# Kernel tuning notes

Measured on AMD Instinct MI355X. Metric: run time of the kernel, lower is better.

Reference implementation:

```python
import jax, jax.numpy as jnp
import numpy as np

H = 1024   # hidden_size
NH = 32    # num_heads
D = H // NH  # head_dim = 32
M = 2      # num_timescales
BMIN, BMAX = 0.85, 0.9995
EPS = 1e-6
ROPE_BASE = 10000.0
LN_EPS = 1e-5


def setup_inputs() -> dict:
    key = jax.random.key(0)
    ks = jax.random.split(key, 8)
    b, t = 4, 1024
    x = jax.random.normal(ks[0], (b, t, H), jnp.float32)
    # xavier-uniform for q/k/v/out (matches _reset_parameters)
    sc = (6.0 / (H + H)) ** 0.5
    Wq = jax.random.uniform(ks[1], (H, H), jnp.float32, -sc, sc)
    Wk = jax.random.uniform(ks[2], (H, H), jnp.float32, -sc, sc)
    Wv = jax.random.uniform(ks[3], (H, H), jnp.float32, -sc, sc)
    Wout = jax.random.uniform(ks[4], (H, H), jnp.float32, -sc, sc)
    bout = jnp.zeros((H,), jnp.float32)
    # beta_proj: random weight, bias set so sigmoid(bias) = linspace(beta_min, beta_max)
    scb = (6.0 / (H + NH * M)) ** 0.5
    Wbeta = jax.random.uniform(ks[5], (NH * M, H), jnp.float32, -scb, scb)
    targets = jnp.linspace(BMIN, BMAX, M)
    bbeta = jnp.tile(jnp.log(targets / (1.0 - targets)), NH)  # repeat 'm -> (h m)'
    # mix_proj initialized to zeros (uniform mixing via softmax)
    Wmix = jnp.zeros((NH * M, H), jnp.float32)
    bmix = jnp.zeros((NH * M,), jnp.float32)
    ln_g = jnp.ones((H,), jnp.float32)
    ln_b = jnp.zeros((H,), jnp.float32)
    return dict(x=x, Wq=Wq, Wk=Wk, Wv=Wv, Wbeta=Wbeta, bbeta=bbeta,
                Wmix=Wmix, bmix=bmix, Wout=Wout, bout=bout, ln_g=ln_g, ln_b=ln_b)


def _rope(u, cos, sin):
    # u: [b,t,h,d] with d even; cos/sin: [1,t,1,d//2]
    half = D // 2
    u1, u2 = u[..., :half], u[..., half:]
    return jnp.concatenate([u1 * cos - u2 * sin, u1 * sin + u2 * cos], axis=-1)


def _forward(x, Wq, Wk, Wv, Wbeta, bbeta, Wmix, bmix, Wout, bout, ln_g, ln_b):
    b, t, _ = x.shape
    q = (x @ Wq.T).reshape(b, t, NH, D)
    k = (x @ Wk.T).reshape(b, t, NH, D)
    v = (x @ Wv.T).reshape(b, t, NH, D)
    # RoPE cache
    half = D // 2
    inv_freq = 1.0 / (ROPE_BASE ** (jnp.arange(half, dtype=jnp.float32) / half))
    freqs = jnp.arange(t, dtype=jnp.float32)[:, None] * inv_freq  # [t,half]
    cos = jnp.cos(freqs)[None, :, None, :]
    sin = jnp.sin(freqs)[None, :, None, :]
    q = _rope(q, cos, sin)
    k = _rope(k, cos, sin)
    phi_q = jax.nn.elu(q) + 1.0
    phi_k = jax.nn.elu(k) + 1.0
    beta = jnp.clip(jax.nn.sigmoid((x @ Wbeta.T + bbeta).reshape(b, t, NH, M)), BMIN, BMAX)
    mix = jax.nn.softmax((x @ Wmix.T + bmix).reshape(b, t, NH, M), axis=-1)

    def step(carry, xs):
        S, K = carry  # S:[b,h,M,d,d]  K:[b,h,M,d]
        pq, pk, vt, bt, mt = xs  # [b,h,d],[b,h,d],[b,h,d],[b,h,M],[b,h,M]
        K = K * bt[..., None] + pk[:, :, None, :]
        S = S * bt[..., None, None] + pk[:, :, None, :, None] * vt[:, :, None, None, :]
        num = jnp.einsum('bhd,bhmdc->bhmc', pq, S)
        den = jnp.einsum('bhd,bhmd->bhm', pq, K) + EPS
        y = jnp.sum(num / den[..., None] * mt[..., None], axis=2)  # [b,h,d]
        return (S, K), y

    S0 = jnp.zeros((b, NH, M, D, D), x.dtype)
    K0 = jnp.zeros((b, NH, M, D), x.dtype)
    tf = lambda a: jnp.moveaxis(a, 1, 0)  # time-major for scan
    _, ys = jax.lax.scan(step, (S0, K0), (tf(phi_q), tf(phi_k), tf(v), tf(beta), tf(mix)))
    y = jnp.moveaxis(ys, 0, 1).reshape(b, t, H) @ Wout.T + bout
    z = x + y  # residual; dropout is identity in eval
    mu = z.mean(-1, keepdims=True)
    var = ((z - mu) ** 2).mean(-1, keepdims=True)
    return (z - mu) / jnp.sqrt(var + LN_EPS) * ln_g + ln_b


def reference(x, Wq, Wk, Wv, Wbeta, bbeta, Wmix, bmix, Wout, bout, ln_g, ln_b):
    return _forward(x, Wq, Wk, Wv, Wbeta, bbeta, Wmix, bmix, Wout, bout, ln_g, ln_b)
```

## Files before the change

kernel.cpp:

```cpp
#include <hip/hip_runtime.h>
#include <math.h>

#define TT 1024
#define BB 4
#define HH 1024
#define NHH 32
#define CL 64
#define NCH (TT/CL)

typedef unsigned short u16;
typedef __attribute__((ext_vector_type(8))) short short8;
typedef __attribute__((ext_vector_type(8))) unsigned short u16x8;
typedef __attribute__((ext_vector_type(4))) float floatx4;

__device__ __forceinline__ float sigmoidf_(float x){ return 1.f/(1.f+expf(-x)); }
__device__ __forceinline__ u16 f2b(float f){
  union { float f; unsigned u; } x; x.f = f;
  unsigned r = x.u + 0x7FFFu + ((x.u >> 16) & 1u);
  return (u16)(r >> 16);
}
__device__ __forceinline__ float b2f(u16 v){
  union { unsigned u; float f; } x; x.u = ((unsigned)v) << 16;
  return x.f;
}

__global__ __launch_bounds__(256) void cast_all_k(
    const float* __restrict__ x, const float* __restrict__ Wq, const float* __restrict__ Wk,
    const float* __restrict__ Wv, const float* __restrict__ Wbeta, const float* __restrict__ Wmix,
    const float* __restrict__ Wout,
    u16* __restrict__ x_bf, u16* __restrict__ Wf, u16* __restrict__ Wout_bf,
    float* __restrict__ ct, float* __restrict__ st)
{
  int gid = blockIdx.x*256 + threadIdx.x;
  if (gid < 16384) {
    int t = gid >> 4, j = gid & 15;
    float invf = powf(10000.f, -(float)j/16.f);
    float ang = (float)t * invf;
    ct[gid] = cosf(ang);
    st[gid] = sinf(ang);
  }
  size_t e = (size_t)gid*4;
  const float* src; u16* dst; size_t so, dof;
  if      (e < 4194304) { src=x;     dst=x_bf;    so=e;          dof=so; }
  else if (e < 5242880) { src=Wq;    dst=Wf;      so=e-4194304;  dof=so; }
  else if (e < 6291456) { src=Wk;    dst=Wf;      so=e-5242880;  dof=so+1048576; }
  else if (e < 7340032) { src=Wv;    dst=Wf;      so=e-6291456;  dof=so+2097152; }
  else if (e < 7405568) { src=Wbeta; dst=Wf;      so=e-7340032;  dof=so+3145728; }
  else if (e < 7471104) { src=Wmix;  dst=Wf;      so=e-7405568;  dof=so+3211264; }
  else                  { src=Wout;  dst=Wout_bf; so=e-7471104;  dof=so; }
  float4 f = *reinterpret_cast<const float4*>(src + so);
  ushort4 u; u.x=f2b(f.x); u.y=f2b(f.y); u.z=f2b(f.z); u.w=f2b(f.w);
  *reinterpret_cast<ushort4*>(dst + dof) = u;
}

__global__ __launch_bounds__(256) void gemm_qkv_k(
    const u16* __restrict__ A, const u16* __restrict__ W,
    const float* __restrict__ ct, const float* __restrict__ st,
    const float* __restrict__ bbeta, const float* __restrict__ bmix,
    u16* __restrict__ qkv, float* __restrict__ betag, float* __restrict__ mixg)
{
  __shared__ u16 As[128*64];
  __shared__ u16 Ws[128*64];
  const int tid = threadIdx.x;
  const int lane = tid & 63;
  const int wave = tid >> 6;
  const int wm = wave >> 1, wn = wave & 1;
  const int id = blockIdx.x;
  const int row0 = (id & 31)*128, bx = id >> 5, col0 = bx*128;
  const int lr = lane & 15, lkg = lane >> 4;

  floatx4 acc[4][4];
  #pragma unroll
  for (int mt=0; mt<4; ++mt)
    #pragma unroll
    for (int nt=0; nt<4; ++nt)
      acc[mt][nt] = (floatx4){0.f,0.f,0.f,0.f};

  for (int k0 = 0; k0 < 1024; k0 += 64) {
    __syncthreads();
    #pragma unroll
    for (int it = 0; it < 4; ++it) {
      int li  = it*256 + tid;
      int row = li >> 3, ckp = li & 7;
      int ck  = ckp ^ (row & 7);
      const u16* ga = A + (size_t)(row0+row)*1024 + k0 + ck*8;
      const u16* gw = W + (size_t)(col0+row)*1024 + k0 + ck*8;
      __builtin_amdgcn_global_load_lds(
          (const __attribute__((address_space(1))) void*)ga,
          (__attribute__((address_space(3))) void*)(As + (size_t)(li & ~63)*8), 16, 0, 0);
      __builtin_amdgcn_global_load_lds(
          (const __attribute__((address_space(1))) void*)gw,
          (__attribute__((address_space(3))) void*)(Ws + (size_t)(li & ~63)*8), 16, 0, 0);
    }
    __syncthreads();
    #pragma unroll
    for (int kk = 0; kk < 64; kk += 32) {
      short8 af[4], wf[4];
      const int ckw = (kk >> 3) + lkg;
      #pragma unroll
      for (int t = 0; t < 4; ++t) {
        int rowA = wm*64 + t*16 + lr;
        int rowW = wn*64 + t*16 + lr;
        af[t] = *reinterpret_cast<const short8*>(As + rowA*64 + (ckw ^ (rowA & 7))*8);
        wf[t] = *reinterpret_cast<const short8*>(Ws + rowW*64 + (ckw ^ (rowW & 7))*8);
      }
      #pragma unroll
      for (int mt = 0; mt < 4; ++mt)
        #pragma unroll
        for (int nt = 0; nt < 4; ++nt)
          acc[mt][nt] = __builtin_amdgcn_mfma_f32_16x16x32_bf16(af[mt], wf[nt], acc[mt][nt], 0, 0, 0);
    }
  }
  if (bx < 16) {
    #pragma unroll
    for (int mt = 0; mt < 4; ++mt) {
      #pragma unroll
      for (int r = 0; r < 4; ++r) {
        int row = row0 + wm*64 + mt*16 + lkg*4 + r;
        int t = row & (TT-1);
        float c_ = ct[t*16 + lr], s_ = st[t*16 + lr];
        #pragma unroll
        for (int nt = 0; nt < 4; nt += 2) {
          float u1 = acc[mt][nt][r], u2 = acc[mt][nt+1][r];
          float r1 = u1*c_ - u2*s_;
          float r2 = u1*s_ + u2*c_;
          r1 = r1 > 0.f ? r1+1.f : expf(r1);
          r2 = r2 > 0.f ? r2+1.f : expf(r2);
          int col = col0 + wn*64 + nt*16 + lr;
          qkv[(size_t)row*3072 + col]      = f2b(r1);
          qkv[(size_t)row*3072 + col + 16] = f2b(r2);
        }
      }
    }
  } else if (bx < 24) {
    #pragma unroll
    for (int mt = 0; mt < 4; ++mt)
      #pragma unroll
      for (int r = 0; r < 4; ++r) {
        int row = row0 + wm*64 + mt*16 + lkg*4 + r;
        #pragma unroll
        for (int nt = 0; nt < 4; ++nt) {
          int col = col0 + wn*64 + nt*16 + lr;
          qkv[(size_t)row*3072 + col] = f2b(acc[mt][nt][r]);
        }
      }
  } else {
    #pragma unroll
    for (int mt = 0; mt < 4; ++mt)
      #pragma unroll
      for (int r = 0; r < 4; ++r) {
        int row = row0 + wm*64 + mt*16 + lkg*4 + r;
        #pragma unroll
        for (int nt = 0; nt < 4; ++nt) {
          int cidx = nt*16 + lr;
          float v = acc[mt][nt][r];
          if (wn == 0) {
            float bv = sigmoidf_(v + bbeta[cidx]);
            betag[(size_t)row*64 + cidx] = fminf(fmaxf(bv, 0.85f), 0.9995f);
          } else {
            float a = v + bmix[cidx];
            float o = __shfl_xor(a, 1);
            float e = expf(a - fmaxf(a, o));
            float es = e + __shfl_xor(e, 1);
            mixg[(size_t)row*64 + cidx] = e/es;
          }
        }
      }
  }
}

__global__ __launch_bounds__(256) void gemm_out_k(
    const u16* __restrict__ A, const u16* __restrict__ W,
    float* __restrict__ Zp0, float* __restrict__ Zp1)
{
  __shared__ u16 As[128*64];
  __shared__ u16 Ws[128*64];
  const int tid = threadIdx.x;
  const int lane = tid & 63;
  const int wave = tid >> 6;
  const int wm = wave >> 1, wn = wave & 1;
  const int id = blockIdx.x;
  const int row0 = (id & 31)*128, col0 = ((id >> 5) & 7)*128, kh = id >> 8;
  float* Z = kh ? Zp1 : Zp0;
  const int lr = lane & 15, lkg = lane >> 4;
  floatx4 acc[4][4];
  #pragma unroll
  for (int mt=0; mt<4; ++mt)
    #pragma unroll
    for (int nt=0; nt<4; ++nt)
      acc[mt][nt] = (floatx4){0.f,0.f,0.f,0.f};
  for (int k0 = kh*512; k0 < kh*512 + 512; k0 += 64) {
    __syncthreads();
    #pragma unroll
    for (int it = 0; it < 4; ++it) {
      int li  = it*256 + tid;
      int row = li >> 3, ckp = li & 7;
      int ck  = ckp ^ (row & 7);
      const u16* ga = A + (size_t)(row0+row)*1024 + k0 + ck*8;
      const u16* gw = W + (size_t)(col0+row)*1024 + k0 + ck*8;
      __builtin_amdgcn_global_load_lds(
          (const __attribute__((address_space(1))) void*)ga,
          (__attribute__((address_space(3))) void*)(As + (size_t)(li & ~63)*8), 16, 0, 0);
      __builtin_amdgcn_global_load_lds(
          (const __attribute__((address_space(1))) void*)gw,
          (__attribute__((address_space(3))) void*)(Ws + (size_t)(li & ~63)*8), 16, 0, 0);
    }
    __syncthreads();
    #pragma unroll
    for (int kk = 0; kk < 64; kk += 32) {
      short8 af[4], wf[4];
      const int ckw = (kk >> 3) + lkg;
      #pragma unroll
      for (int t = 0; t < 4; ++t) {
        int rowA = wm*64 + t*16 + lr;
        int rowW = wn*64 + t*16 + lr;
        af[t] = *reinterpret_cast<const short8*>(As + rowA*64 + (ckw ^ (rowA & 7))*8);
        wf[t] = *reinterpret_cast<const short8*>(Ws + rowW*64 + (ckw ^ (rowW & 7))*8);
      }
      #pragma unroll
      for (int mt = 0; mt < 4; ++mt)
        #pragma unroll
        for (int nt = 0; nt < 4; ++nt)
          acc[mt][nt] = __builtin_amdgcn_mfma_f32_16x16x32_bf16(af[mt], wf[nt], acc[mt][nt], 0, 0, 0);
    }
  }
  #pragma unroll
  for (int mt = 0; mt < 4; ++mt)
    #pragma unroll
    for (int r = 0; r < 4; ++r) {
      int row = row0 + wm*64 + mt*16 + lkg*4 + r;
      #pragma unroll
      for (int nt = 0; nt < 4; ++nt) {
        int col = col0 + wn*64 + nt*16 + lr;
        Z[(size_t)row*HH + col] = acc[mt][nt][r];
      }
    }
}

__global__ __launch_bounds__(256) void scan_delta_k(
    const u16* __restrict__ qkv, const float* __restrict__ betag,
    float* __restrict__ dS, float* __restrict__ dK,
    float* __restrict__ pLg, float* __restrict__ pg)
{
  __shared__ __align__(16) u16 K2T[2][32][72];
  __shared__ __align__(16) u16 VT[32][72];
  __shared__ float bets[2][64], pbuf[2][64], wjs[2][64], pLs[2];
  const int ch = blockIdx.x, h = blockIdx.y, b = blockIdx.z;
  const int bh = b*NHH + h;
  const int tid = threadIdx.x;
  const int t0 = ch*CL;
  const int j = tid >> 2, oct = tid & 3;
  size_t rowbase = (size_t)(b*TT + t0 + j)*3072 + h*32 + oct*8;
  u16x8 k8 = *reinterpret_cast<const u16x8*>(qkv + rowbase + 1024);
  u16x8 v8 = *reinterpret_cast<const u16x8*>(qkv + rowbase + 2048);
  if (tid < 128) {
    int m = tid & 1, tl = tid >> 1;
    bets[m][tl] = betag[(size_t)(b*TT + t0 + tl)*64 + h*2 + m];
  }
  #pragma unroll
  for (int dd = 0; dd < 8; ++dd) VT[oct*8+dd][j] = v8[dd];
  __syncthreads();
  if (tid < 128) {
    int m = tid >> 6, l = tid & 63;
    float p = bets[m][l];
    #pragma unroll
    for (int off = 1; off < 64; off <<= 1) {
      float o = __shfl_up(p, off);
      if (l >= off) p *= o;
    }
    pbuf[m][l] = p;
    if (l == 63) pLs[m] = p;
  }
  __syncthreads();
  if (tid < 128) {
    int m = tid >> 6, l = tid & 63;
    wjs[m][l] = pLs[m] / pbuf[m][l];
    pg[(((size_t)bh*NCH + ch)*2 + m)*64 + l] = pbuf[m][l];
  }
  if (tid < 2) pLg[((size_t)bh*NCH + ch)*2 + tid] = pLs[tid];
  __syncthreads();
  float w0 = wjs[0][j], w1 = wjs[1][j];
  #pragma unroll
  for (int dd = 0; dd < 8; ++dd) {
    float kv = b2f(k8[dd]);
    K2T[0][oct*8+dd][j] = f2b(kv*w0);
    K2T[1][oct*8+dd][j] = f2b(kv*w1);
  }
  __syncthreads();
  {
    const int wv = tid >> 6, lane = tid & 63, lr = lane & 15, kg = lane >> 4;
    const int m = wv >> 1, mt = wv & 1;
    floatx4 a0 = (floatx4){0.f,0.f,0.f,0.f}, a1 = (floatx4){0.f,0.f,0.f,0.f};
    #pragma unroll
    for (int ks = 0; ks < 2; ++ks) {
      short8 af = *reinterpret_cast<const short8*>(&K2T[m][mt*16 + lr][ks*32 + kg*8]);
      short8 b0 = *reinterpret_cast<const short8*>(&VT[lr][ks*32 + kg*8]);
      short8 b1 = *reinterpret_cast<const short8*>(&VT[16 + lr][ks*32 + kg*8]);
      a0 = __builtin_amdgcn_mfma_f32_16x16x32_bf16(af, b0, a0, 0, 0, 0);
      a1 = __builtin_amdgcn_mfma_f32_16x16x32_bf16(af, b1, a1, 0, 0, 0);
    }
    size_t base = (((size_t)bh*NCH + ch)*2 + m)*1024;
    #pragma unroll
    for (int r = 0; r < 4; ++r) {
      int d = mt*16 + kg*4 + r;
      dS[base + d*32 + lr]      = a0[r];
      dS[base + d*32 + 16 + lr] = a1[r];
    }
  }
  if (tid < 64) {
    int m = tid >> 5, d = tid & 31;
    float s = 0.f;
    #pragma unroll
    for (int g = 0; g < 8; ++g) {
      u16x8 kk = *reinterpret_cast<const u16x8*>(&K2T[m][d][g*8]);
      #pragma unroll
      for (int dd = 0; dd < 8; ++dd) s += b2f(kk[dd]);
    }
    dK[(((size_t)bh*NCH + ch)*2 + m)*32 + d] = s;
  }
}

__global__ __launch_bounds__(256) void scan_state_k(
    float* dSS0, float* dKK0, const float* __restrict__ pLg)
{
  const int bhm = blockIdx.x >> 2, part = blockIdx.x & 3;
  const int bh = bhm >> 1, m = bhm & 1;
  const int idx = part*256 + threadIdx.x;
  float pls[NCH], dv[NCH];
  #pragma unroll
  for (int ch = 0; ch < NCH; ++ch) pls[ch] = pLg[((size_t)bh*NCH + ch)*2 + m];
  #pragma unroll
  for (int ch = 0; ch < NCH; ++ch) dv[ch] = dSS0[(((size_t)bh*NCH + ch)*2 + m)*1024 + idx];
  float S = 0.f;
  #pragma unroll
  for (int ch = 0; ch < NCH; ++ch) {
    dSS0[(((size_t)bh*NCH + ch)*2 + m)*1024 + idx] = S;
    S = fmaf(pls[ch], S, dv[ch]);
  }
  if (part == 0 && threadIdx.x < 32) {
    int d = threadIdx.x;
    float kv[NCH];
    #pragma unroll
    for (int ch = 0; ch < NCH; ++ch) kv[ch] = dKK0[(((size_t)bh*NCH + ch)*2 + m)*32 + d];
    float K0 = 0.f;
    #pragma unroll
    for (int ch = 0; ch < NCH; ++ch) {
      dKK0[(((size_t)bh*NCH + ch)*2 + m)*32 + d] = K0;
      K0 = fmaf(pls[ch], K0, kv[ch]);
    }
  }
}

__global__ __launch_bounds__(256) void scan_apply_k(
    const u16* __restrict__ qkv, const float* __restrict__ mixg,
    const float* __restrict__ S0g, const float* __restrict__ K0g,
    const float* __restrict__ pg, u16* __restrict__ yb)
{
  __shared__ __align__(16) u16 Qs[64][32], Ks[64][32];
  __shared__ __align__(16) u16 VT[32][72];
  __shared__ __align__(16) u16 At[2][64][72];
  __shared__ __align__(16) u16 S0T[2][2][32][40];
  __shared__ float K0s[2][32];
  __shared__ float pbv[2][64], ipb[2][64], mixs[2][64], coef[2][64];
  const int ch = blockIdx.x, h = blockIdx.y, b = blockIdx.z;
  const int bh = b*NHH + h;
  const int tid = threadIdx.x;
  const int t0 = ch*CL;
  {
    int j = tid >> 2, oct = tid & 3;
    size_t rb = (size_t)(b*TT + t0 + j)*3072 + h*32 + oct*8;
    u16x8 q8 = *reinterpret_cast<const u16x8*>(qkv + rb);
    u16x8 k8 = *reinterpret_cast<const u16x8*>(qkv + rb + 1024);
    u16x8 v8 = *reinterpret_cast<const u16x8*>(qkv + rb + 2048);
    *reinterpret_cast<u16x8*>(&Qs[j][oct*8]) = q8;
    *reinterpret_cast<u16x8*>(&Ks[j][oct*8]) = k8;
    #pragma unroll
    for (int dd = 0; dd < 8; ++dd) VT[oct*8+dd][j] = v8[dd];
  }
  for (int u = tid; u < 2048; u += 256) {
    int m = u >> 10, r = u & 1023, d = r >> 5, c = r & 31;
    float val = S0g[(((size_t)bh*NCH + ch)*2 + m)*1024 + r];
    u16 hv = f2b(val);
    float lo = val - b2f(hv);
    S0T[m][0][c][d] = hv;
    S0T[m][1][c][d] = f2b(lo);
  }
  if (tid < 64) {
    int m = tid >> 5, d = tid & 31;
    K0s[m][d] = K0g[(((size_t)bh*NCH + ch)*2 + m)*32 + d];
  }
  if (tid < 128) {
    int m = tid & 1, i = tid >> 1;
    float p = pg[(((size_t)bh*NCH + ch)*2 + m)*64 + i];
    pbv[m][i] = p;
    ipb[m][i] = 1.f/p;
  } else if (tid < 192) {
    int i = tid - 128;
    size_t rb = (size_t)(b*TT + t0 + i)*64 + h*2;
    mixs[0][i] = mixg[rb];
    mixs[1][i] = mixg[rb+1];
  }
  __syncthreads();
  {
    const int wv = tid >> 6, lane = tid & 63, lr = lane & 15, kg = lane >> 4;
    short8 aq = *reinterpret_cast<const short8*>(&Qs[wv*16 + lr][kg*8]);
    #pragma unroll
    for (int nt = 0; nt < 4; ++nt) {
      short8 bk = *reinterpret_cast<const short8*>(&Ks[nt*16 + lr][kg*8]);
      floatx4 a0 = (floatx4){0.f,0.f,0.f,0.f};
      a0 = __builtin_amdgcn_mfma_f32_16x16x32_bf16(aq, bk, a0, 0, 0, 0);
      int jg = nt*16 + lr;
      float ip0 = ipb[0][jg], ip1 = ipb[1][jg];
      #pragma unroll
      for (int r = 0; r < 4; ++r) {
        int ig = wv*16 + kg*4 + r;
        float val = a0[r];
        bool ok = (jg <= ig);
        At[0][ig][jg] = f2b(ok ? val*ip0 : 0.f);
        At[1][ig][jg] = f2b(ok ? val*ip1 : 0.f);
      }
    }
  }
  __syncthreads();
  if (tid < 128) {
    int m = tid & 1, i = tid >> 1;
    float qK0 = 0.f;
    #pragma unroll
    for (int g = 0; g < 4; ++g) {
      u16x8 qq = *reinterpret_cast<const u16x8*>(&Qs[i][g*8]);
      #pragma unroll
      for (int dd = 0; dd < 8; ++dd) qK0 = fmaf(b2f(qq[dd]), K0s[m][g*8+dd], qK0);
    }
    float As_ = 0.f;
    #pragma unroll
    for (int g = 0; g < 8; ++g) {
      u16x8 aa = *reinterpret_cast<const u16x8*>(&At[m][i][g*8]);
      #pragma unroll
      for (int dd = 0; dd < 8; ++dd) As_ += b2f(aa[dd]);
    }
    float den = pbv[m][i]*(qK0 + As_) + 1e-6f;
    coef[m][i] = mixs[m][i]*pbv[m][i]/den;
  }
  __syncthreads();
  {
    const int wv = tid >> 6, lane = tid & 63, lr = lane & 15, kg = lane >> 4;
    const int i0 = wv*16;
    floatx4 accY[2][2];
    #pragma unroll
    for (int m = 0; m < 2; ++m)
      #pragma unroll
      for (int nt = 0; nt < 2; ++nt)
        accY[m][nt] = (floatx4){0.f,0.f,0.f,0.f};
    short8 aq = *reinterpret_cast<const short8*>(&Qs[i0 + lr][kg*8]);
    #pragma unroll
    for (int m = 0; m < 2; ++m)
      #pragma unroll
      for (int nt = 0; nt < 2; ++nt) {
        short8 bhi = *reinterpret_cast<const short8*>(&S0T[m][0][nt*16 + lr][kg*8]);
        short8 blo = *reinterpret_cast<const short8*>(&S0T[m][1][nt*16 + lr][kg*8]);
        accY[m][nt] = __builtin_amdgcn_mfma_f32_16x16x32_bf16(aq, bhi, accY[m][nt], 0, 0, 0);
        accY[m][nt] = __builtin_amdgcn_mfma_f32_16x16x32_bf16(aq, blo, accY[m][nt], 0, 0, 0);
      }
    #pragma unroll
    for (int ks = 0; ks < 2; ++ks) {
      short8 a0f = *reinterpret_cast<const short8*>(&At[0][i0 + lr][ks*32 + kg*8]);
      short8 a1f = *reinterpret_cast<const short8*>(&At[1][i0 + lr][ks*32 + kg*8]);
      short8 b0 = *reinterpret_cast<const short8*>(&VT[lr][ks*32 + kg*8]);
      short8 b1 = *reinterpret_cast<const short8*>(&VT[16 + lr][ks*32 + kg*8]);
      accY[0][0] = __builtin_amdgcn_mfma_f32_16x16x32_bf16(a0f, b0, accY[0][0], 0, 0, 0);
      accY[0][1] = __builtin_amdgcn_mfma_f32_16x16x32_bf16(a0f, b1, accY[0][1], 0, 0, 0);
      accY[1][0] = __builtin_amdgcn_mfma_f32_16x16x32_bf16(a1f, b0, accY[1][0], 0, 0, 0);
      accY[1][1] = __builtin_amdgcn_mfma_f32_16x16x32_bf16(a1f, b1, accY[1][1], 0, 0, 0);
    }
    #pragma unroll
    for (int r = 0; r < 4; ++r) {
      int i = i0 + kg*4 + r;
      float c0 = coef[0][i], c1 = coef[1][i];
      size_t ob = (size_t)(b*TT + t0 + i)*HH + h*32;
      yb[ob + lr]      = f2b(c0*accY[0][0][r] + c1*accY[1][0][r]);
      yb[ob + 16 + lr] = f2b(c0*accY[0][1][r] + c1*accY[1][1][r]);
    }
  }
}

__global__ __launch_bounds__(256) void ln_k(
    const float* __restrict__ xr, const float* __restrict__ zp0, const float* __restrict__ zp1,
    const float* __restrict__ bout, const float* __restrict__ g,
    const float* __restrict__ bta, float* __restrict__ out)
{
  const int row = blockIdx.x;
  const int tid = threadIdx.x;
  size_t o = (size_t)row*HH/4 + tid;
  float4 xv = reinterpret_cast<const float4*>(xr)[o];
  float4 z0 = reinterpret_cast<const float4*>(zp0)[o];
  float4 z1 = reinterpret_cast<const float4*>(zp1)[o];
  float4 bo = reinterpret_cast<const float4*>(bout)[tid];
  float4 zv;
  zv.x = xv.x + z0.x + z1.x + bo.x;
  zv.y = xv.y + z0.y + z1.y + bo.y;
  zv.z = xv.z + z0.z + z1.z + bo.z;
  zv.w = xv.w + z0.w + z1.w + bo.w;
  float sum = zv.x+zv.y+zv.z+zv.w;
  float sq  = zv.x*zv.x + zv.y*zv.y + zv.z*zv.z + zv.w*zv.w;
  #pragma unroll
  for (int off=1; off<64; off<<=1){ sum += __shfl_xor(sum, off); sq += __shfl_xor(sq, off); }
  __shared__ float s1[4], s2[4];
  int w = tid>>6;
  if ((tid&63)==0){ s1[w]=sum; s2[w]=sq; }
  __syncthreads();
  sum = s1[0]+s1[1]+s1[2]+s1[3];
  sq  = s2[0]+s2[1]+s2[2]+s2[3];
  float mu  = sum * (1.f/1024.f);
  float var = sq * (1.f/1024.f) - mu*mu;
  float rstd = rsqrtf(var + 1e-5f);
  float4 gv = reinterpret_cast<const float4*>(g)[tid];
  float4 bv = reinterpret_cast<const float4*>(bta)[tid];
  float4 ov;
  ov.x = (zv.x-mu)*rstd*gv.x + bv.x;
  ov.y = (zv.y-mu)*rstd*gv.y + bv.y;
  ov.z = (zv.z-mu)*rstd*gv.z + bv.z;
  ov.w = (zv.w-mu)*rstd*gv.w + bv.w;
  reinterpret_cast<float4*>(out)[o] = ov;
}

extern "C" void kernel_launch(void* const* d_in, const int* in_sizes, int n_in,
                              void* d_out, int out_size, void* d_ws, size_t ws_size,
                              hipStream_t stream)
{
  const float* x     = (const float*)d_in[0];
  const float* Wq    = (const float*)d_in[1];
  const float* Wk    = (const float*)d_in[2];
  const float* Wv    = (const float*)d_in[3];
  const float* Wbeta = (const float*)d_in[4];
  const float* bbeta = (const float*)d_in[5];
  const float* Wmix  = (const float*)d_in[6];
  const float* bmix  = (const float*)d_in[7];
  const float* Wout  = (const float*)d_in[8];
  const float* bout  = (const float*)d_in[9];
  const float* ln_g  = (const float*)d_in[10];
  const float* ln_b  = (const float*)d_in[11];
  float* out = (float*)d_out;

  float* ws = (float*)d_ws;
  float* ct      = ws;
  float* st      = ws + 16384;
  u16*   x_bf    = (u16*)(ws + 32768);
  u16*   Wf      = (u16*)(ws + 2129920);
  u16*   Wout_bf = (u16*)(ws + 3768320);
  u16*   qkv     = (u16*)(ws + 4292608);
  float* betag   = ws + 10584064;
  float* mixg    = ws + 10846208;
  float* dSS0    = ws + 11108352;
  float* dKK0    = ws + 15302656;
  float* pLg     = ws + 15433728;
  float* pg      = ws + 15437824;
  u16*   y_bf    = x_bf;
  float* zp0     = dSS0;
  float* zp1     = (float*)qkv;

  cast_all_k<<<8320, 256, 0, stream>>>(x, Wq, Wk, Wv, Wbeta, Wmix, Wout,
                                       x_bf, Wf, Wout_bf, ct, st);
  gemm_qkv_k<<<800, 256, 0, stream>>>(x_bf, Wf, ct, st, bbeta, bmix, qkv, betag, mixg);
  dim3 gscan(NCH, 32, 4);
  scan_delta_k<<<gscan, 256, 0, stream>>>(qkv, betag, dSS0, dKK0, pLg, pg);
  scan_state_k<<<1024, 256, 0, stream>>>(dSS0, dKK0, pLg);
  scan_apply_k<<<gscan, 256, 0, stream>>>(qkv, mixg, dSS0, dKK0, pg, y_bf);
  gemm_out_k<<<512, 256, 0, stream>>>(y_bf, Wout_bf, zp0, zp1);
  ln_k<<<4096, 256, 0, stream>>>(x, zp0, zp1, bout, ln_g, ln_b, out);
}
```

Baseline: 224.4 us.

## Drop split-K in output GEMM, fuse residual and bias into its epilogue

The output projection GEMM no longer splits K into two halves written to separate partial buffers. Each block now computes a full-K 128x64 tile with a single-row wave layout and adds the bias and residual x directly in the epilogue. The layernorm kernel then reads a single z buffer instead of three arrays plus the bias. Both GEMMs also get a launch-bounds minimum-occupancy hint of 5. This removes one full-size partial write and two reads but halves the MFMA work per block and doubles its K loop, which could lower arithmetic intensity.

```diff
diff --git a/kernel.cpp b/kernel.cpp
--- a/kernel.cpp
+++ b/kernel.cpp
@@ -53,7 +53,7 @@
   *reinterpret_cast<ushort4*>(dst + dof) = u;
 }
 
-__global__ __launch_bounds__(256) void gemm_qkv_k(
+__global__ __launch_bounds__(256, 5) void gemm_qkv_k(
     const u16* __restrict__ A, const u16* __restrict__ W,
     const float* __restrict__ ct, const float* __restrict__ st,
     const float* __restrict__ bbeta, const float* __restrict__ bmix,
@@ -169,27 +169,26 @@
   }
 }
 
-__global__ __launch_bounds__(256) void gemm_out_k(
+__global__ __launch_bounds__(256, 5) void gemm_out_k(
     const u16* __restrict__ A, const u16* __restrict__ W,
-    float* __restrict__ Zp0, float* __restrict__ Zp1)
+    const float* __restrict__ xr, const float* __restrict__ bout,
+    float* __restrict__ Z)
 {
   __shared__ u16 As[128*64];
-  __shared__ u16 Ws[128*64];
+  __shared__ u16 Ws[64*64];
   const int tid = threadIdx.x;
   const int lane = tid & 63;
   const int wave = tid >> 6;
-  const int wm = wave >> 1, wn = wave & 1;
   const int id = blockIdx.x;
-  const int row0 = (id & 31)*128, col0 = ((id >> 5) & 7)*128, kh = id >> 8;
-  float* Z = kh ? Zp1 : Zp0;
+  const int row0 = (id & 31)*128, col0 = (id >> 5)*64;
   const int lr = lane & 15, lkg = lane >> 4;
-  floatx4 acc[4][4];
-  #pragma unroll
-  for (int mt=0; mt<4; ++mt)
+  floatx4 acc[2][4];
+  #pragma unroll
+  for (int mt=0; mt<2; ++mt)
     #pragma unroll
     for (int nt=0; nt<4; ++nt)
       acc[mt][nt] = (floatx4){0.f,0.f,0.f,0.f};
-  for (int k0 = kh*512; k0 < kh*512 + 512; k0 += 64) {
+  for (int k0 = 0; k0 < 1024; k0 += 64) {
     __syncthreads();
     #pragma unroll
     for (int it = 0; it < 4; ++it) {
@@ -197,10 +196,16 @@
       int row = li >> 3, ckp = li & 7;
       int ck  = ckp ^ (row & 7);
       const u16* ga = A + (size_t)(row0+row)*1024 + k0 + ck*8;
-      const u16* gw = W + (size_t)(col0+row)*1024 + k0 + ck*8;
       __builtin_amdgcn_global_load_lds(
           (const __attribute__((address_space(1))) void*)ga,
           (__attribute__((address_space(3))) void*)(As + (size_t)(li & ~63)*8), 16, 0, 0);
+    }
+    #pragma unroll
+    for (int it = 0; it < 2; ++it) {
+      int li  = it*256 + tid;
+      int row = li >> 3, ckp = li & 7;
+      int ck  = ckp ^ (row & 7);
+      const u16* gw = W + (size_t)(col0+row)*1024 + k0 + ck*8;
       __builtin_amdgcn_global_load_lds(
           (const __attribute__((address_space(1))) void*)gw,
           (__attribute__((address_space(3))) void*)(Ws + (size_t)(li & ~63)*8), 16, 0, 0);
@@ -208,31 +213,34 @@
     __syncthreads();
     #pragma unroll
     for (int kk = 0; kk < 64; kk += 32) {
-      short8 af[4], wf[4];
+      short8 af[2], wf[4];
       const int ckw = (kk >> 3) + lkg;
       #pragma unroll
+      for (int t = 0; t < 2; ++t) {
+        int rowA = wave*32 + t*16 + lr;
+        af[t] = *reinterpret_cast<const short8*>(As + rowA*64 + (ckw ^ (rowA & 7))*8);
+      }
+      #pragma unroll
       for (int t = 0; t < 4; ++t) {
-        int rowA = wm*64 + t*16 + lr;
-        int rowW = wn*64 + t*16 + lr;
-        af[t] = *reinterpret_cast<const short8*>(As + rowA*64 + (ckw ^ (rowA & 7))*8);
+        int rowW = t*16 + lr;
         wf[t] = *reinterpret_cast<const short8*>(Ws + rowW*64 + (ckw ^ (rowW & 7))*8);
       }
       #pragma unroll
-      for (int mt = 0; mt < 4; ++mt)
+      for (int mt = 0; mt < 2; ++mt)
         #pragma unroll
         for (int nt = 0; nt < 4; ++nt)
           acc[mt][nt] = __builtin_amdgcn_mfma_f32_16x16x32_bf16(af[mt], wf[nt], acc[mt][nt], 0, 0, 0);
     }
   }
   #pragma unroll
-  for (int mt = 0; mt < 4; ++mt)
+  for (int mt = 0; mt < 2; ++mt)
     #pragma unroll
     for (int r = 0; r < 4; ++r) {
-      int row = row0 + wm*64 + mt*16 + lkg*4 + r;
+      int row = row0 + wave*32 + mt*16 + lkg*4 + r;
       #pragma unroll
       for (int nt = 0; nt < 4; ++nt) {
-        int col = col0 + wn*64 + nt*16 + lr;
-        Z[(size_t)row*HH + col] = acc[mt][nt][r];
+        int col = col0 + nt*16 + lr;
+        Z[(size_t)row*HH + col] = acc[mt][nt][r] + bout[col] + xr[(size_t)row*HH + col];
       }
     }
 }
@@ -484,22 +492,13 @@
 }
 
 __global__ __launch_bounds__(256) void ln_k(
-    const float* __restrict__ xr, const float* __restrict__ zp0, const float* __restrict__ zp1,
-    const float* __restrict__ bout, const float* __restrict__ g,
+    const float* __restrict__ z, const float* __restrict__ g,
     const float* __restrict__ bta, float* __restrict__ out)
 {
   const int row = blockIdx.x;
   const int tid = threadIdx.x;
   size_t o = (size_t)row*HH/4 + tid;
-  float4 xv = reinterpret_cast<const float4*>(xr)[o];
-  float4 z0 = reinterpret_cast<const float4*>(zp0)[o];
-  float4 z1 = reinterpret_cast<const float4*>(zp1)[o];
-  float4 bo = reinterpret_cast<const float4*>(bout)[tid];
-  float4 zv;
-  zv.x = xv.x + z0.x + z1.x + bo.x;
-  zv.y = xv.y + z0.y + z1.y + bo.y;
-  zv.z = xv.z + z0.z + z1.z + bo.z;
-  zv.w = xv.w + z0.w + z1.w + bo.w;
+  float4 zv = reinterpret_cast<const float4*>(z)[o];
   float sum = zv.x+zv.y+zv.z+zv.w;
   float sq  = zv.x*zv.x + zv.y*zv.y + zv.z*zv.z + zv.w*zv.w;
   #pragma unroll
@@ -555,8 +554,7 @@
   float* pLg     = ws + 15433728;
   float* pg      = ws + 15437824;
   u16*   y_bf    = x_bf;
-  float* zp0     = dSS0;
-  float* zp1     = (float*)qkv;
+  float* z       = dSS0;
 
   cast_all_k<<<8320, 256, 0, stream>>>(x, Wq, Wk, Wv, Wbeta, Wmix, Wout,
                                        x_bf, Wf, Wout_bf, ct, st);
@@ -565,6 +563,6 @@
   scan_delta_k<<<gscan, 256, 0, stream>>>(qkv, betag, dSS0, dKK0, pLg, pg);
   scan_state_k<<<1024, 256, 0, stream>>>(dSS0, dKK0, pLg);
   scan_apply_k<<<gscan, 256, 0, stream>>>(qkv, mixg, dSS0, dKK0, pg, y_bf);
-  gemm_out_k<<<512, 256, 0, stream>>>(y_bf, Wout_bf, zp0, zp1);
-  ln_k<<<4096, 256, 0, stream>>>(x, zp0, zp1, bout, ln_g, ln_b, out);
-}
+  gemm_out_k<<<512, 256, 0, stream>>>(y_bf, Wout_bf, x, bout, z);
+  ln_k<<<4096, 256, 0, stream>>>(z, ln_g, ln_b, out);
+}
```

New measurement: 258.5 us. +15.2%, slower.
